# Kernel optimization log

Measured on AMD Instinct MI355X. Metric: run time of the kernel, lower is better.

Reference implementation:

```python
import jax, jax.numpy as jnp
import numpy as np

# Nemotron-H Mamba2 mixer decoder layer (prefill path, zero initial states,
# full context lengths). Dims per init_kwargs.
B, S, H = 1, 256, 4096
NH, P, G, N, K = 128, 64, 8, 128, 4   # num_heads, head_dim, n_groups, ssm_state_size, conv_kernel
D_INNER = NH * P                      # 8192
D_STATE = G * N                       # 1024
CONV_DIM = D_INNER + 2 * D_STATE      # 10240
IN_OUT = D_INNER + CONV_DIM + NH      # 18560
EPS = 1e-6


def setup_inputs() -> dict:
    key = jax.random.key(0)
    ks = jax.random.split(key, 8)
    sc = 0.02
    return {
        "hidden_states": jax.random.normal(ks[0], (B, S, H), jnp.float32),
        "conv_state": jnp.zeros((B, CONV_DIM, K - 1), jnp.float32),
        "ssm_state": jnp.zeros((B, NH, P, N), jnp.float32),
        "norm_weight": jnp.ones((H,), jnp.float32),
        "w_in": jax.random.normal(ks[1], (IN_OUT, H), jnp.float32) * sc,
        "conv_w": jax.random.normal(ks[2], (CONV_DIM, K), jnp.float32) * 0.2,
        "conv_b": jnp.zeros((CONV_DIM,), jnp.float32),
        "A_log": jax.random.uniform(ks[3], (NH,), jnp.float32, 0.0, 1.0),
        "D_param": jax.random.normal(ks[4], (NH,), jnp.float32) * 0.1,
        "dt_bias": jax.random.normal(ks[5], (NH,), jnp.float32) * 0.1,
        "ssm_norm_weight": jnp.ones((D_INNER,), jnp.float32),
        "w_out": jax.random.normal(ks[6], (H, D_INNER), jnp.float32) * sc,
    }


def _rmsnorm(x, w, eps=EPS):
    var = jnp.mean(x * x, axis=-1, keepdims=True)
    return x * jax.lax.rsqrt(var + eps) * w


def reference(hidden_states, conv_state, ssm_state, norm_weight, w_in, conv_w,
              conv_b, A_log, D_param, dt_bias, ssm_norm_weight, w_out):
    resid = hidden_states
    h = _rmsnorm(hidden_states, norm_weight)           # pre-mixer RMSNorm
    proj = jnp.einsum('bsh,oh->bso', h, w_in)          # in_proj [B,S,18560]
    gate = proj[..., :D_INNER]
    xconv = proj[..., D_INNER:D_INNER + CONV_DIM]
    dt = proj[..., D_INNER + CONV_DIM:]                # [B,S,NH]

    # depthwise causal conv1d, initial left context = conv_state
    xc = jnp.swapaxes(xconv, 1, 2)                     # [B,CONV_DIM,S]
    xpad = jnp.concatenate([conv_state, xc], axis=-1)  # [B,CONV_DIM,S+K-1]
    conv_state_out = xpad[:, :, -(K - 1):]
    y = conv_b[None, :, None]
    for j in range(K):                                 # K=4 taps, unrolled
        y = y + conv_w[:, j][None, :, None] * xpad[:, :, j:j + S]
    y = jax.nn.silu(jnp.swapaxes(y, 1, 2))             # [B,S,CONV_DIM]

    xs = y[..., :D_INNER].reshape(B, S, NH, P)
    Bs = y[..., D_INNER:D_INNER + D_STATE].reshape(B, S, G, N)
    Cs = y[..., D_INNER + D_STATE:].reshape(B, S, G, N)

    A = -jnp.exp(A_log)                                # [NH]
    dtp = jax.nn.softplus(dt + dt_bias)                # [B,S,NH]
    rep = NH // G
    Bh = jnp.repeat(Bs, rep, axis=2)                   # [B,S,NH,N]
    Ch = jnp.repeat(Cs, rep, axis=2)

    def step(state, inp):
        x_t, b_t, c_t, dt_t = inp                      # [B,NH,P],[B,NH,N],[B,NH,N],[B,NH]
        dA = jnp.exp(dt_t * A)                         # [B,NH]
        state = state * dA[..., None, None] + (dt_t[..., None] * x_t)[..., None] * b_t[:, :, None, :]
        y_t = jnp.einsum('bhpn,bhn->bhp', state, c_t)
        return state, y_t

    inps = (jnp.swapaxes(xs, 0, 1), jnp.swapaxes(Bh, 0, 1),
            jnp.swapaxes(Ch, 0, 1), jnp.swapaxes(dtp, 0, 1))
    ssm_state_out, ys = jax.lax.scan(step, ssm_state, inps)
    ys = jnp.swapaxes(ys, 0, 1) + D_param[None, None, :, None] * xs
    ssm_out = ys.reshape(B, S, D_INNER)

    # gated grouped RMSNorm (group_size = D_INNER // G = 1024)
    gated = ssm_out * jax.nn.silu(gate)
    gsize = D_INNER // G
    gg = gated.reshape(B, S, D_INNER // gsize, gsize)
    var = jnp.mean(gg * gg, axis=-1, keepdims=True)
    normed = (gg * jax.lax.rsqrt(var + EPS)).reshape(B, S, D_INNER) * ssm_norm_weight

    out = jnp.einsum('bsd,hd->bsh', normed, w_out)     # out_proj
    return resid + out, conv_state_out, ssm_state_out
```

## Files before the change

### kernel.cpp

```cpp
#include <hip/hip_runtime.h>
#include <hip/hip_bf16.h>

#define Sq 256
#define Hd 4096
#define NH 128
#define Pd 64
#define Gg 8
#define Nn 128
#define D_INNER 8192
#define D_STATE 1024
#define CONV_DIM 10240
#define IN_OUT 18560
#define DT_COL0 18432
#define EPSI 1e-6f

typedef _Float16 f16x8 __attribute__((ext_vector_type(8)));
typedef _Float16 f16x2 __attribute__((ext_vector_type(2)));
typedef float f32x4 __attribute__((ext_vector_type(4)));

__device__ inline ushort f2h(float f) {
  _Float16 h = (_Float16)f;
  return __builtin_bit_cast(ushort, h);
}
__device__ inline ushort f2h_lo(float f, ushort hi) {
  float hf = (float)__builtin_bit_cast(_Float16, hi);
  _Float16 l = (_Float16)(f - hf);
  return __builtin_bit_cast(ushort, l);
}
__device__ inline f16x2 pkrtz(float a, float b) {
  return __builtin_bit_cast(f16x2, __builtin_amdgcn_cvt_pkrtz(a, b));
}

__global__ __launch_bounds__(256) void rmsnorm_k(const float* __restrict__ x,
                                                 const float* __restrict__ w,
                                                 ushort* __restrict__ h_hi,
                                                 ushort* __restrict__ h_lo) {
  int s = blockIdx.x, t = threadIdx.x;
  const float4* row = reinterpret_cast<const float4*>(x + (size_t)s * Hd);
  const float4* wv  = reinterpret_cast<const float4*>(w);
  float4 v[4];
  float ss = 0.f;
#pragma unroll
  for (int i = 0; i < 4; i++) {
    v[i] = row[t + i * 256];
    ss += v[i].x * v[i].x + v[i].y * v[i].y + v[i].z * v[i].z + v[i].w * v[i].w;
  }
#pragma unroll
  for (int off = 32; off > 0; off >>= 1) ss += __shfl_xor(ss, off);
  __shared__ float red[4];
  if ((t & 63) == 0) red[t >> 6] = ss;
  __syncthreads();
  ss = red[0] + red[1] + red[2] + red[3];
  float scale = rsqrtf(ss * (1.f / (float)Hd) + EPSI);
  ushort4* hh = reinterpret_cast<ushort4*>(h_hi + (size_t)s * Hd);
  ushort4* hl = reinterpret_cast<ushort4*>(h_lo + (size_t)s * Hd);
#pragma unroll
  for (int i = 0; i < 4; i++) {
    float4 wi = wv[t + i * 256];
    float f0 = v[i].x * scale * wi.x, f1 = v[i].y * scale * wi.y;
    float f2 = v[i].z * scale * wi.z, f3 = v[i].w * scale * wi.w;
    ushort4 oh, ol;
    oh.x = f2h(f0); ol.x = f2h_lo(f0, oh.x);
    oh.y = f2h(f1); ol.y = f2h_lo(f1, oh.y);
    oh.z = f2h(f2); ol.z = f2h_lo(f2, oh.z);
    oh.w = f2h(f3); ol.w = f2h_lo(f3, oh.w);
    hh[t + i * 256] = oh;
    hl[t + i * 256] = ol;
  }
}

__global__ __launch_bounds__(512) void gemm_gl(const ushort* __restrict__ A,
                                               const float* __restrict__ B,
                                               float* __restrict__ C,
                                               int ldc, int K, int kLen) {
  __shared__ __align__(16) ushort As[2][256 * 32];
  __shared__ __align__(16) float  Bsf[2][64 * 32];
  int t = threadIdx.x;
  int wave = t >> 6, lane = t & 63;
  int wr = wave & 3, wc = wave >> 2;
  int frow = lane & 15;
  int gq = lane >> 4;
  int bcol = blockIdx.x * 64;
  int kStart = blockIdx.z * kLen;
  C += (size_t)blockIdx.z * Sq * ldc;

  int ar = t >> 2;
  int aq = (t & 3) ^ (ar & 3);
  const ushort* ApG0 = A + (size_t)ar * K + kStart + aq * 8;
  const ushort* ApG1 = ApG0 + (size_t)128 * K;
  int br = t >> 3;
  int bq = (t & 7) ^ (br & 7);
  const float* BpG = B + (size_t)(bcol + br) * K + kStart + bq * 4;

  char* dstA0 = (char*)&As[0][0] + wave * 1024;
  char* dstA1 = (char*)&As[0][0] + 8192 + wave * 1024;
  char* dstB  = (char*)&Bsf[0][0] + wave * 1024;

  f32x4 acc[4][2] = {};

#define STAGE(p, kk) { \
    __builtin_amdgcn_global_load_lds( \
        (const __attribute__((address_space(1))) void*)(ApG0 + (kk)), \
        (__attribute__((address_space(3))) void*)(dstA0 + (p) * 16384), 16, 0, 0); \
    __builtin_amdgcn_global_load_lds( \
        (const __attribute__((address_space(1))) void*)(ApG1 + (kk)), \
        (__attribute__((address_space(3))) void*)(dstA1 + (p) * 16384), 16, 0, 0); \
    __builtin_amdgcn_global_load_lds( \
        (const __attribute__((address_space(1))) void*)(BpG + (kk)), \
        (__attribute__((address_space(3))) void*)(dstB + (p) * 8192), 16, 0, 0); }

  STAGE(0, 0)
  __syncthreads();
  int cur = 0;
  for (int ki = 0; ki < kLen; ki += 32) {
    if (ki + 32 < kLen) STAGE(cur ^ 1, ki + 32)
    f16x8 af[4], bf[2];
#pragma unroll
    for (int m = 0; m < 4; ++m) {
      int row = wr * 64 + m * 16 + frow;
      af[m] = *(const f16x8*)((const char*)&As[cur][0] + row * 64 + ((gq ^ (frow & 3)) * 16));
    }
#pragma unroll
    for (int n = 0; n < 2; ++n) {
      int row = wc * 32 + n * 16 + frow;
      int g0 = 2 * gq, r7 = frow & 7;
      float4 b0 = *(const float4*)((const char*)&Bsf[cur][0] + row * 128 + ((g0 ^ r7) * 16));
      float4 b1 = *(const float4*)((const char*)&Bsf[cur][0] + row * 128 + (((g0 + 1) ^ r7) * 16));
      union { f16x2 h2[4]; f16x8 h8; } u;
      u.h2[0] = pkrtz(b0.x, b0.y);
      u.h2[1] = pkrtz(b0.z, b0.w);
      u.h2[2] = pkrtz(b1.x, b1.y);
      u.h2[3] = pkrtz(b1.z, b1.w);
      bf[n] = u.h8;
    }
#pragma unroll
    for (int m = 0; m < 4; ++m)
#pragma unroll
      for (int n = 0; n < 2; ++n)
        acc[m][n] = __builtin_amdgcn_mfma_f32_16x16x32_f16(af[m], bf[n], acc[m][n], 0, 0, 0);
    __syncthreads();
    cur ^= 1;
  }
#undef STAGE

#pragma unroll
  for (int m = 0; m < 4; ++m) {
    int row0 = wr * 64 + m * 16 + (lane >> 4) * 4;
#pragma unroll
    for (int n = 0; n < 2; ++n) {
      int col = bcol + wc * 32 + n * 16 + frow;
#pragma unroll
      for (int r = 0; r < 4; ++r)
        C[(size_t)(row0 + r) * ldc + col] = acc[m][n][r];
    }
  }
}

template<int BN, bool SPLIT>
__global__ __launch_bounds__(256) void gemm_mfma(const ushort* __restrict__ A_hi,
                                                 const ushort* __restrict__ A_lo,
                                                 const float* __restrict__ B,
                                                 float* __restrict__ C,
                                                 int ldc, int K, int kLen,
                                                 int bcol0, int M) {
  constexpr int BK = 64;
  constexpr int LDA = 72;
  constexpr int N_REP = BN / 32;
  constexpr int BQN = (BN == 128) ? 8 : 4;
  __shared__ __align__(16) ushort As[64 * LDA];
  __shared__ __align__(16) ushort Bs[BN * LDA];
  __shared__ __align__(16) ushort AsL[SPLIT ? 64 * LDA : 1];
  __shared__ __align__(16) ushort BsL[SPLIT ? BN * LDA : 1];

  int t = threadIdx.x;
  int wave = t >> 6, lane = t & 63;
  int wr = wave >> 1, wc = wave & 1;
  int frow = lane & 15, fk = (lane >> 4) * 8;
  int rowBase = blockIdx.x * 64;
  int bcol = bcol0 + blockIdx.y * BN;
  int ccol = blockIdx.y * BN;
  int kStart = blockIdx.z * kLen;
  C += (size_t)blockIdx.z * M * ldc;

  int arow = t >> 2, ak = (t & 3) * 16;
  const ushort* Ap  = A_hi + (size_t)(rowBase + arow) * K + ak;
  const ushort* ApL = SPLIT ? (A_lo + (size_t)(rowBase + arow) * K + ak) : nullptr;

  int brow, bq;
  if constexpr (BN == 128) { brow = t >> 1; bq = (t & 1) * 32; }
  else                     { brow = t >> 2; bq = (t & 3) * 16; }
  const float* Bp = B + (size_t)(bcol + brow) * K + bq;

  f32x4 acc[2][N_REP] = {};
  uint4 aPre[2], aPreL[2];
  float4 bPre[BQN];

  auto loadK = [&](int kk) {
    aPre[0] = *reinterpret_cast<const uint4*>(Ap + kk);
    aPre[1] = *reinterpret_cast<const uint4*>(Ap + kk + 8);
    if constexpr (SPLIT) {
      aPreL[0] = *reinterpret_cast<const uint4*>(ApL + kk);
      aPreL[1] = *reinterpret_cast<const uint4*>(ApL + kk + 8);
    }
#pragma unroll
    for (int j = 0; j < BQN; ++j)
      bPre[j] = *reinterpret_cast<const float4*>(Bp + kk + j * 4);
  };

  loadK(kStart);
  for (int ki = 0; ki < kLen; ki += BK) {
    __syncthreads();
    *reinterpret_cast<uint4*>(&As[arow * LDA + ak])     = aPre[0];
    *reinterpret_cast<uint4*>(&As[arow * LDA + ak + 8]) = aPre[1];
    if constexpr (SPLIT) {
      *reinterpret_cast<uint4*>(&AsL[arow * LDA + ak])     = aPreL[0];
      *reinterpret_cast<uint4*>(&AsL[arow * LDA + ak + 8]) = aPreL[1];
    }
    {
      ushort hb[BQN * 4];
      ushort lb[SPLIT ? BQN * 4 : 1];
      const float* bf = reinterpret_cast<const float*>(bPre);
#pragma unroll
      for (int j = 0; j < BQN * 4; ++j) {
        hb[j] = f2h(bf[j]);
        if constexpr (SPLIT) lb[j] = f2h_lo(bf[j], hb[j]);
      }
#pragma unroll
      for (int j = 0; j < BQN / 2; ++j)
        *reinterpret_cast<uint4*>(&Bs[brow * LDA + bq + j * 8]) =
            reinterpret_cast<const uint4*>(hb)[j];
      if constexpr (SPLIT) {
#pragma unroll
        for (int j = 0; j < BQN / 2; ++j)
          *reinterpret_cast<uint4*>(&BsL[brow * LDA + bq + j * 8]) =
              reinterpret_cast<const uint4*>(lb)[j];
      }
    }
    __syncthreads();
    if (ki + BK < kLen) loadK(kStart + ki + BK);
    f16x8 af[2][2], bfv[N_REP][2];
    f16x8 afL[SPLIT ? 2 : 1][2], bfL[SPLIT ? N_REP : 1][2];
#pragma unroll
    for (int m = 0; m < 2; ++m)
#pragma unroll
      for (int kh = 0; kh < 2; ++kh) {
        af[m][kh] = *reinterpret_cast<const f16x8*>(
            &As[(wr * 32 + m * 16 + frow) * LDA + kh * 32 + fk]);
        if constexpr (SPLIT)
          afL[m][kh] = *reinterpret_cast<const f16x8*>(
              &AsL[(wr * 32 + m * 16 + frow) * LDA + kh * 32 + fk]);
      }
#pragma unroll
    for (int n = 0; n < N_REP; ++n)
#pragma unroll
      for (int kh = 0; kh < 2; ++kh) {
        bfv[n][kh] = *reinterpret_cast<const f16x8*>(
            &Bs[(wc * (BN / 2) + n * 16 + frow) * LDA + kh * 32 + fk]);
        if constexpr (SPLIT)
          bfL[n][kh] = *reinterpret_cast<const f16x8*>(
              &BsL[(wc * (BN / 2) + n * 16 + frow) * LDA + kh * 32 + fk]);
      }
#pragma unroll
    for (int kh = 0; kh < 2; ++kh)
#pragma unroll
      for (int m = 0; m < 2; ++m)
#pragma unroll
        for (int n = 0; n < N_REP; ++n) {
          acc[m][n] = __builtin_amdgcn_mfma_f32_16x16x32_f16(af[m][kh], bfv[n][kh], acc[m][n], 0, 0, 0);
          if constexpr (SPLIT) {
            acc[m][n] = __builtin_amdgcn_mfma_f32_16x16x32_f16(af[m][kh], bfL[n][kh], acc[m][n], 0, 0, 0);
            acc[m][n] = __builtin_amdgcn_mfma_f32_16x16x32_f16(afL[m][kh], bfv[n][kh], acc[m][n], 0, 0, 0);
          }
        }
  }

#pragma unroll
  for (int m = 0; m < 2; ++m) {
    int row0 = rowBase + wr * 32 + m * 16 + (lane >> 4) * 4;
#pragma unroll
    for (int n = 0; n < N_REP; ++n) {
      int col = ccol + wc * (BN / 2) + n * 16 + frow;
#pragma unroll
      for (int r = 0; r < 4; ++r)
        C[(size_t)(row0 + r) * ldc + col] = acc[m][n][r];
    }
  }
}

__global__ __launch_bounds__(256) void reduce2_k(float* __restrict__ p0,
                                                 const float* __restrict__ p1) {
  int i = blockIdx.x * 256 + threadIdx.x;
  float4 a = reinterpret_cast<const float4*>(p0)[i];
  float4 b = reinterpret_cast<const float4*>(p1)[i];
  a.x += b.x; a.y += b.y; a.z += b.z; a.w += b.w;
  reinterpret_cast<float4*>(p0)[i] = a;
}

__global__ __launch_bounds__(256) void conv_silu_k(const float* __restrict__ proj,
                                                   const float* __restrict__ cstate,
                                                   const float* __restrict__ cw,
                                                   const float* __restrict__ cb,
                                                   float* __restrict__ y) {
  int c = blockIdx.x * 256 + threadIdx.x;
  int s = blockIdx.y;
  float acc = cb[c];
  float4 w4 = *reinterpret_cast<const float4*>(cw + c * 4);
  float wj[4] = {w4.x, w4.y, w4.z, w4.w};
#pragma unroll
  for (int j = 0; j < 4; j++) {
    int si = s + j - 3;
    float v = (si < 0) ? cstate[c * 3 + (si + 3)]
                       : proj[(size_t)si * IN_OUT + D_INNER + c];
    acc += wj[j] * v;
  }
  float sig = 1.f / (1.f + expf(-acc));
  y[(size_t)s * CONV_DIM + c] = acc * sig;
}

__global__ __launch_bounds__(256) void conv_state_out_k(const float* __restrict__ proj,
                                                        float* __restrict__ out1) {
  int idx = blockIdx.x * 256 + threadIdx.x;
  int c = idx / 3, tt = idx % 3;
  out1[idx] = proj[(size_t)(Sq - 3 + tt) * IN_OUT + D_INNER + c];
}

__global__ __launch_bounds__(256) void dt_k(const float* __restrict__ dtfix,
                                            const float* __restrict__ dt_bias,
                                            float* __restrict__ dtp) {
  int idx = blockIdx.x * 256 + threadIdx.x;
  int hh = idx & 127;
  float v = dtfix[idx] + dtfix[32768 + idx] + dtfix[65536 + idx] + dtfix[98304 + idx]
            + dt_bias[hh];
  dtp[idx] = (v > 20.f) ? v : log1pf(expf(v));
}

#define CS 16
__global__ __launch_bounds__(256) void ssm_scan_k(const float* __restrict__ y_conv,
                                                  const float* __restrict__ dtp,
                                                  const float* __restrict__ sstate_in,
                                                  const float* __restrict__ A_log,
                                                  const float* __restrict__ D_param,
                                                  float* __restrict__ ys_out,
                                                  float* __restrict__ sstate_out) {
  int h = blockIdx.x >> 1;
  int pb = (blockIdx.x & 1) * 32;
  int t = threadIdx.x;
  int ng = t & 7, pl = t >> 3;
  int g = h >> 4;
  float A = -expf(A_log[h]);
  float Dp = D_param[h];

  float st[16];
  {
    const float* sp = sstate_in + ((size_t)h * Pd + pb + pl) * Nn + ng * 16;
#pragma unroll
    for (int i = 0; i < 16; i += 4) {
      float4 v = *reinterpret_cast<const float4*>(sp + i);
      st[i] = v.x; st[i + 1] = v.y; st[i + 2] = v.z; st[i + 3] = v.w;
    }
  }

  __shared__ float ybuf[CS][296];
  __shared__ float dts[CS];
  int lr = t >> 4;
  int lc = t & 15;

  for (int ch = 0; ch < Sq / CS; ++ch) {
    int s0 = ch * CS;
    __syncthreads();
    const float* rowp = y_conv + (size_t)(s0 + lr) * CONV_DIM;
#pragma unroll
    for (int j = 0; j < 5; ++j) {
      int c = lc + 16 * j;
      if (c < 72) {
        const float* src;
        if (c < 8)       src = rowp + h * 64 + pb + c * 4;
        else if (c < 40) src = rowp + D_INNER + g * 128 + (c - 8) * 4;
        else             src = rowp + D_INNER + D_STATE + g * 128 + (c - 40) * 4;
        *reinterpret_cast<float4*>(&ybuf[lr][c * 4]) = *reinterpret_cast<const float4*>(src);
      }
    }
    if (t < CS) dts[t] = dtp[(s0 + t) * NH + h];
    __syncthreads();

#pragma unroll 4
    for (int stp = 0; stp < CS; ++stp) {
      float dt = dts[stp];
      float dA = expf(dt * A);
      float x0 = ybuf[stp][pl];
      float dtx = dt * x0;
      float y0 = 0.f;
#pragma unroll
      for (int i = 0; i < 16; ++i) {
        float b = ybuf[stp][32 + ng * 16 + i];
        float c = ybuf[stp][160 + ng * 16 + i];
        st[i] = st[i] * dA + dtx * b;
        y0 += st[i] * c;
      }
      y0 += __shfl_xor(y0, 1); y0 += __shfl_xor(y0, 2); y0 += __shfl_xor(y0, 4);
      if (ng == 0)
        ys_out[(size_t)(s0 + stp) * D_INNER + h * 64 + pb + pl] = y0 + Dp * x0;
    }
  }

  float* so = sstate_out + ((size_t)h * Pd + pb + pl) * Nn + ng * 16;
#pragma unroll
  for (int i = 0; i < 16; i += 4)
    *reinterpret_cast<float4*>(so + i) = make_float4(st[i], st[i + 1], st[i + 2], st[i + 3]);
}

__global__ __launch_bounds__(256) void gated_norm_k(const float* __restrict__ ys,
                                                    const float* __restrict__ proj,
                                                    const float* __restrict__ w,
                                                    ushort* __restrict__ out_h) {
  int s = blockIdx.x, g = blockIdx.y, t = threadIdx.x;
  float vals[4];
  float ss = 0.f;
#pragma unroll
  for (int i = 0; i < 4; i++) {
    int d = g * 1024 + i * 256 + t;
    float gate = proj[(size_t)s * IN_OUT + d];
    float v = ys[(size_t)s * D_INNER + d] * (gate / (1.f + expf(-gate)));
    vals[i] = v;
    ss += v * v;
  }
#pragma unroll
  for (int off = 32; off > 0; off >>= 1) ss += __shfl_xor(ss, off);
  __shared__ float red[4];
  if ((t & 63) == 0) red[t >> 6] = ss;
  __syncthreads();
  ss = red[0] + red[1] + red[2] + red[3];
  float scale = rsqrtf(ss * (1.f / 1024.f) + EPSI);
#pragma unroll
  for (int i = 0; i < 4; i++) {
    int d = g * 1024 + i * 256 + t;
    out_h[(size_t)s * D_INNER + d] = f2h(vals[i] * scale * w[d]);
  }
}

__global__ __launch_bounds__(256) void reduce_out_k(const float* __restrict__ p,
                                                    const float* __restrict__ hidden,
                                                    float* __restrict__ out0) {
  int i = blockIdx.x * 256 + threadIdx.x;
  const int PL = Sq * Hd / 4;
  float4 o = reinterpret_cast<const float4*>(hidden)[i];
#pragma unroll
  for (int z = 0; z < 8; ++z) {
    float4 a = reinterpret_cast<const float4*>(p)[i + z * PL];
    o.x += a.x; o.y += a.y; o.z += a.z; o.w += a.w;
  }
  reinterpret_cast<float4*>(out0)[i] = o;
}

extern "C" void kernel_launch(void* const* d_in, const int* in_sizes, int n_in,
                              void* d_out, int out_size, void* d_ws, size_t ws_size,
                              hipStream_t stream) {
  const float* hidden    = (const float*)d_in[0];
  const float* cstate_in = (const float*)d_in[1];
  const float* sstate_in = (const float*)d_in[2];
  const float* norm_w    = (const float*)d_in[3];
  const float* w_in      = (const float*)d_in[4];
  const float* conv_w    = (const float*)d_in[5];
  const float* conv_b    = (const float*)d_in[6];
  const float* A_log     = (const float*)d_in[7];
  const float* D_param   = (const float*)d_in[8];
  const float* dt_bias   = (const float*)d_in[9];
  const float* ssm_nw    = (const float*)d_in[10];
  const float* w_out     = (const float*)d_in[11];

  float* out0 = (float*)d_out;
  float* out1 = out0 + (size_t)Sq * Hd;
  float* out2 = out1 + (size_t)CONV_DIM * 3;

  ushort* h_hi  = (ushort*)d_ws;
  ushort* h_lo  = h_hi + (size_t)Sq * Hd;
  float* proj   = (float*)(h_lo + (size_t)Sq * Hd);
  float* y_conv = proj + (size_t)Sq * IN_OUT;
  float* dtp    = y_conv + (size_t)Sq * CONV_DIM;
  float* ys     = dtp + (size_t)Sq * NH;
  ushort* ys_h  = (ushort*)(ys + (size_t)Sq * D_INNER);
  float* dtfix  = (float*)(ys_h + (size_t)Sq * D_INNER);
  float* oppart = proj;

  rmsnorm_k<<<Sq, 256, 0, stream>>>(hidden, norm_w, h_hi, h_lo);
  gemm_gl<<<dim3(IN_OUT / 64, 1, 2), 512, 0, stream>>>(h_hi, w_in, proj, IN_OUT, Hd, Hd / 2);
  reduce2_k<<<(Sq * IN_OUT / 4) / 256, 256, 0, stream>>>(proj, proj + (size_t)Sq * IN_OUT);
  gemm_mfma<64, true><<<dim3(4, 2, 4), 256, 0, stream>>>(
      h_hi, h_lo, w_in, dtfix, NH, Hd, Hd / 4, DT_COL0, Sq);
  conv_silu_k<<<dim3(CONV_DIM / 256, Sq), 256, 0, stream>>>(proj, cstate_in, conv_w, conv_b, y_conv);
  conv_state_out_k<<<(CONV_DIM * 3) / 256, 256, 0, stream>>>(proj, out1);
  dt_k<<<(Sq * NH) / 256, 256, 0, stream>>>(dtfix, dt_bias, dtp);
  ssm_scan_k<<<NH * 2, 256, 0, stream>>>(y_conv, dtp, sstate_in, A_log, D_param, ys, out2);
  gated_norm_k<<<dim3(Sq, Gg), 256, 0, stream>>>(ys, proj, ssm_nw, ys_h);
  gemm_gl<<<dim3(Hd / 64, 1, 8), 512, 0, stream>>>(ys_h, w_out, oppart, Hd, D_INNER, D_INNER / 8);
  reduce_out_k<<<(Sq * Hd / 4) / 256, 256, 0, stream>>>(oppart, hidden, out0);
}
```

Measured before the change: 386.8 us.

## Replace GEMM with 128x128 tiles, converting B to fp16 once in LDS

Replaces the 256x64-tile, 512-thread GEMM with a 128x128-tile, 256-thread kernel in which each block covers half the rows of a 128-column tile. The fp32 weights are now loaded into registers, converted to fp16 once, and written to LDS. Previously the raw fp32 was staged and every wave re-converted it on each read. The change aims to halve LDS traffic for B, remove redundant conversions, and give each wave more MFMAs per fragment load. The cost is more register pressure and twice as many weight reads from global memory per column, since two blocks now share each column tile.

```diff
diff --git a/kernel.cpp b/kernel.cpp
--- a/kernel.cpp
+++ b/kernel.cpp
@@ -69,86 +69,100 @@
   }
 }
 
-__global__ __launch_bounds__(512) void gemm_gl(const ushort* __restrict__ A,
-                                               const float* __restrict__ B,
-                                               float* __restrict__ C,
-                                               int ldc, int K, int kLen) {
-  __shared__ __align__(16) ushort As[2][256 * 32];
-  __shared__ __align__(16) float  Bsf[2][64 * 32];
+__global__ __launch_bounds__(256, 3) void gemm_t128(const ushort* __restrict__ A,
+                                                    const float* __restrict__ B,
+                                                    float* __restrict__ C,
+                                                    int ldc, int K, int kLen) {
+  __shared__ __align__(16) ushort As[2][128 * 32];
+  __shared__ __align__(16) ushort Bs[2][128 * 32];
   int t = threadIdx.x;
   int wave = t >> 6, lane = t & 63;
-  int wr = wave & 3, wc = wave >> 2;
-  int frow = lane & 15;
-  int gq = lane >> 4;
-  int bcol = blockIdx.x * 64;
+  int wr = wave >> 1, wc = wave & 1;
+  int frow = lane & 15, gq = lane >> 4;
+  int coltile = blockIdx.x >> 1;
+  int rowBase = (blockIdx.x & 1) * 128;
+  int bcol = coltile * 128;
   int kStart = blockIdx.z * kLen;
   C += (size_t)blockIdx.z * Sq * ldc;
 
   int ar = t >> 2;
-  int aq = (t & 3) ^ (ar & 3);
-  const ushort* ApG0 = A + (size_t)ar * K + kStart + aq * 8;
-  const ushort* ApG1 = ApG0 + (size_t)128 * K;
-  int br = t >> 3;
-  int bq = (t & 7) ^ (br & 7);
-  const float* BpG = B + (size_t)(bcol + br) * K + kStart + bq * 4;
-
+  int ax = (ar >> 1) & 3;
+  const ushort* ApG0 = A + (size_t)(rowBase + ar) * K + kStart + ((t & 3) ^ ax) * 8;
+  const ushort* ApG1 = ApG0 + (size_t)64 * K;
   char* dstA0 = (char*)&As[0][0] + wave * 1024;
-  char* dstA1 = (char*)&As[0][0] + 8192 + wave * 1024;
-  char* dstB  = (char*)&Bsf[0][0] + wave * 1024;
-
-  f32x4 acc[4][2] = {};
-
-#define STAGE(p, kk) { \
+  char* dstA1 = (char*)&As[0][0] + 4096 + wave * 1024;
+
+  int brow = t >> 1, bhalf = t & 1;
+  int bx = (brow >> 1) & 3;
+  const float* BpG = B + (size_t)(bcol + brow) * K + kStart + bhalf * 16;
+  int bslot0 = ((2 * bhalf) ^ bx) * 16;
+  int bslot1 = ((2 * bhalf + 1) ^ bx) * 16;
+  float4 rb[4];
+
+  f32x4 acc[4][4] = {};
+  const int NT = kLen / 32;
+
+#define ISSUE_B(kk) { _Pragma("unroll") for (int j = 0; j < 4; ++j) \
+                        rb[j] = *(const float4*)(BpG + (kk) + j * 4); }
+#define DMA_A(p, kk) { \
     __builtin_amdgcn_global_load_lds( \
         (const __attribute__((address_space(1))) void*)(ApG0 + (kk)), \
-        (__attribute__((address_space(3))) void*)(dstA0 + (p) * 16384), 16, 0, 0); \
+        (__attribute__((address_space(3))) void*)(dstA0 + (p) * 8192), 16, 0, 0); \
     __builtin_amdgcn_global_load_lds( \
         (const __attribute__((address_space(1))) void*)(ApG1 + (kk)), \
-        (__attribute__((address_space(3))) void*)(dstA1 + (p) * 16384), 16, 0, 0); \
-    __builtin_amdgcn_global_load_lds( \
-        (const __attribute__((address_space(1))) void*)(BpG + (kk)), \
-        (__attribute__((address_space(3))) void*)(dstB + (p) * 8192), 16, 0, 0); }
-
-  STAGE(0, 0)
+        (__attribute__((address_space(3))) void*)(dstA1 + (p) * 8192), 16, 0, 0); }
+#define WRITE_B(p) { \
+    union { f16x2 h2[8]; uint4 q[2]; } u; \
+    u.h2[0] = pkrtz(rb[0].x, rb[0].y); u.h2[1] = pkrtz(rb[0].z, rb[0].w); \
+    u.h2[2] = pkrtz(rb[1].x, rb[1].y); u.h2[3] = pkrtz(rb[1].z, rb[1].w); \
+    u.h2[4] = pkrtz(rb[2].x, rb[2].y); u.h2[5] = pkrtz(rb[2].z, rb[2].w); \
+    u.h2[6] = pkrtz(rb[3].x, rb[3].y); u.h2[7] = pkrtz(rb[3].z, rb[3].w); \
+    char* bb = (char*)&Bs[0][0] + (p) * 8192 + brow * 64; \
+    *(uint4*)(bb + bslot0) = u.q[0]; \
+    *(uint4*)(bb + bslot1) = u.q[1]; }
+
+  ISSUE_B(0)
+  DMA_A(0, 0)
+  WRITE_B(0)
   __syncthreads();
-  int cur = 0;
-  for (int ki = 0; ki < kLen; ki += 32) {
-    if (ki + 32 < kLen) STAGE(cur ^ 1, ki + 32)
-    f16x8 af[4], bf[2];
+
+  for (int i = 0; i < NT; ++i) {
+    int cur = i & 1;
+    if (i + 1 < NT) {
+      ISSUE_B((i + 1) * 32)
+      DMA_A(cur ^ 1, (i + 1) * 32)
+    }
+    f16x8 af[4], bf[4];
 #pragma unroll
     for (int m = 0; m < 4; ++m) {
       int row = wr * 64 + m * 16 + frow;
-      af[m] = *(const f16x8*)((const char*)&As[cur][0] + row * 64 + ((gq ^ (frow & 3)) * 16));
-    }
-#pragma unroll
-    for (int n = 0; n < 2; ++n) {
-      int row = wc * 32 + n * 16 + frow;
-      int g0 = 2 * gq, r7 = frow & 7;
-      float4 b0 = *(const float4*)((const char*)&Bsf[cur][0] + row * 128 + ((g0 ^ r7) * 16));
-      float4 b1 = *(const float4*)((const char*)&Bsf[cur][0] + row * 128 + (((g0 + 1) ^ r7) * 16));
-      union { f16x2 h2[4]; f16x8 h8; } u;
-      u.h2[0] = pkrtz(b0.x, b0.y);
-      u.h2[1] = pkrtz(b0.z, b0.w);
-      u.h2[2] = pkrtz(b1.x, b1.y);
-      u.h2[3] = pkrtz(b1.z, b1.w);
-      bf[n] = u.h8;
+      af[m] = *(const f16x8*)((const char*)&As[0][0] + cur * 8192 + row * 64 +
+                              ((gq ^ ((row >> 1) & 3)) * 16));
+    }
+#pragma unroll
+    for (int n = 0; n < 4; ++n) {
+      int row = wc * 64 + n * 16 + frow;
+      bf[n] = *(const f16x8*)((const char*)&Bs[0][0] + cur * 8192 + row * 64 +
+                              ((gq ^ ((row >> 1) & 3)) * 16));
     }
 #pragma unroll
     for (int m = 0; m < 4; ++m)
 #pragma unroll
-      for (int n = 0; n < 2; ++n)
+      for (int n = 0; n < 4; ++n)
         acc[m][n] = __builtin_amdgcn_mfma_f32_16x16x32_f16(af[m], bf[n], acc[m][n], 0, 0, 0);
+    if (i + 1 < NT) WRITE_B(cur ^ 1)
     __syncthreads();
-    cur ^= 1;
-  }
-#undef STAGE
+  }
+#undef ISSUE_B
+#undef DMA_A
+#undef WRITE_B
 
 #pragma unroll
   for (int m = 0; m < 4; ++m) {
-    int row0 = wr * 64 + m * 16 + (lane >> 4) * 4;
-#pragma unroll
-    for (int n = 0; n < 2; ++n) {
-      int col = bcol + wc * 32 + n * 16 + frow;
+    int row0 = rowBase + wr * 64 + m * 16 + (lane >> 4) * 4;
+#pragma unroll
+    for (int n = 0; n < 4; ++n) {
+      int col = bcol + wc * 64 + n * 16 + frow;
 #pragma unroll
       for (int r = 0; r < 4; ++r)
         C[(size_t)(row0 + r) * ldc + col] = acc[m][n][r];
@@ -483,7 +497,8 @@
   float* oppart = proj;
 
   rmsnorm_k<<<Sq, 256, 0, stream>>>(hidden, norm_w, h_hi, h_lo);
-  gemm_gl<<<dim3(IN_OUT / 64, 1, 2), 512, 0, stream>>>(h_hi, w_in, proj, IN_OUT, Hd, Hd / 2);
+  gemm_t128<<<dim3(2 * (IN_OUT / 128), 1, 2), 256, 0, stream>>>(
+      h_hi, w_in, proj, IN_OUT, Hd, Hd / 2);
   reduce2_k<<<(Sq * IN_OUT / 4) / 256, 256, 0, stream>>>(proj, proj + (size_t)Sq * IN_OUT);
   gemm_mfma<64, true><<<dim3(4, 2, 4), 256, 0, stream>>>(
       h_hi, h_lo, w_in, dtfix, NH, Hd, Hd / 4, DT_COL0, Sq);
@@ -492,6 +507,7 @@
   dt_k<<<(Sq * NH) / 256, 256, 0, stream>>>(dtfix, dt_bias, dtp);
   ssm_scan_k<<<NH * 2, 256, 0, stream>>>(y_conv, dtp, sstate_in, A_log, D_param, ys, out2);
   gated_norm_k<<<dim3(Sq, Gg), 256, 0, stream>>>(ys, proj, ssm_nw, ys_h);
-  gemm_gl<<<dim3(Hd / 64, 1, 8), 512, 0, stream>>>(ys_h, w_out, oppart, Hd, D_INNER, D_INNER / 8);
+  gemm_t128<<<dim3(2 * (Hd / 128), 1, 8), 256, 0, stream>>>(
+      ys_h, w_out, oppart, Hd, D_INNER, D_INNER / 8);
   reduce_out_k<<<(Sq * Hd / 4) / 256, 256, 0, stream>>>(oppart, hidden, out0);
 }
```

New measurement: 405.7 us. 4.9% more time.
